# Kernel optimization log

Hardware: AMD Instinct MI355X
Metric: run time of the kernel (lower is better)

## Reference

```python
import jax, jax.numpy as jnp
import numpy as np

N = 50000   # nodes
E = 800000  # edges (avg degree 16)
IN = 384    # input gene features
H = 256     # hidden
EPS = 1e-12 # F.normalize eps


def setup_inputs() -> dict:
    key = jax.random.key(0)
    ks = jax.random.split(key, 10)
    x = jax.random.uniform(ks[0], (N, IN), dtype=jnp.float32) * 10.0  # count-like
    src = jax.random.randint(ks[1], (E,), 0, N, dtype=jnp.int32)
    dst = jax.random.randint(ks[2], (E,), 0, N, dtype=jnp.int32)
    def lin(k, din):
        return (jax.random.normal(k, (din, H), dtype=jnp.float32) / np.sqrt(din).astype(np.float32))
    return {
        'x': x, 'src': src, 'dst': dst,
        'W_self0': lin(ks[3], IN), 'W_neigh0': lin(ks[4], IN), 'b0': jnp.zeros((H,), jnp.float32),
        'W_self1': lin(ks[5], H), 'W_neigh1': lin(ks[6], H), 'b1': jnp.zeros((H,), jnp.float32),
        'W_self2': lin(ks[7], H), 'W_neigh2': lin(ks[8], H), 'b2': jnp.zeros((H,), jnp.float32),
    }


def _sage_mean(h, src, dst, Ws, Wn, b):
    # gather neighbor feats along edges, mean-aggregate into dst nodes
    msg = h[src]                                             # [E, d]
    agg = jax.ops.segment_sum(msg, dst, num_segments=N)      # [N, d]
    deg = jax.ops.segment_sum(jnp.ones((E,), h.dtype), dst, num_segments=N)
    h_neigh = agg / jnp.maximum(deg, 1.0)[:, None]           # isolated nodes -> 0
    return h @ Ws + h_neigh @ Wn + b


def _l2norm(h):
    n = jnp.sqrt(jnp.sum(h * h, axis=-1, keepdims=True))
    return h / jnp.maximum(n, EPS)


def reference(x, src, dst, W_self0, W_neigh0, b0, W_self1, W_neigh1, b1, W_self2, W_neigh2, b2):
    h = jnp.log1p(x)
    # layers 0..n-2: SAGEConv -> relu -> L2 normalize
    h = _l2norm(jax.nn.relu(_sage_mean(h, src, dst, W_self0, W_neigh0, b0)))
    h = _l2norm(jax.nn.relu(_sage_mean(h, src, dst, W_self1, W_neigh1, b1)))
    # last layer: plain SAGEConv (feat_drop inactive in eval)
    h = _sage_mean(h, src, dst, W_self2, W_neigh2, b2)
    return h
```

## Files before the change

### kernel.cpp

```cpp
#include <hip/hip_runtime.h>
#include <hip/hip_bf16.h>

#define N_NODES 50000
#define N_EDGES 800000
#define DIM_IN  384
#define DIM_H   256

typedef __bf16 bf16x8 __attribute__((ext_vector_type(8)));
typedef float  f32x4  __attribute__((ext_vector_type(4)));

static __device__ __forceinline__ ushort f2bf(float f) {
  uint u = __float_as_uint(f);
  u += 0x7fffu + ((u >> 16) & 1u);
  return (ushort)(u >> 16);
}
static __device__ __forceinline__ float bf_lo(uint u) { return __uint_as_float(u << 16); }
static __device__ __forceinline__ float bf_hi(uint u) { return __uint_as_float(u & 0xffff0000u); }

typedef const __attribute__((address_space(1))) void* gas_p;
typedef __attribute__((address_space(3))) void* las_p;
static __device__ __forceinline__ void gload16(const void* g, void* l) {
  __builtin_amdgcn_global_load_lds((gas_p)g, (las_p)l, 16, 0, 0);
}

static __device__ __forceinline__ float log1p_fast(float x) {
  return __logf(1.0f + x);
}

static __device__ __forceinline__ int permc(int p) {
  return ((p >> 7) << 7) + ((p & 7) << 4) + ((p >> 3) & 15);
}
static __device__ __forceinline__ void pack_one(const float* W, ushort* out, int local, bool perm) {
  int k = local >> 8, col = local & 255;
  int kc = k >> 5, kgd = (k >> 3) & 3, e = k & 7;
  int kgs = kgd ^ ((col >> 1) & 3);
  int krow = perm ? permc(k) : k;
  out[((size_t)kc * 256 + col) * 32 + kgs * 8 + e] = f2bf(W[krow * 256 + col]);
}

#define HIST_BLOCKS 3125
#define STRIPE1_TOT (HIST_BLOCKS * 7)
#define PACK_TOT (2 * DIM_IN * 256 + 4 * DIM_H * 256)
#define PACK_BLOCKS ((PACK_TOT + 255) / 256)

__global__ void prep_kernel(const float* __restrict__ x, ushort* __restrict__ h,
                            const int* __restrict__ dst, int* __restrict__ deg,
                            const float* W0s, const float* W0n, const float* W1s,
                            const float* W1n, const float* W2s, const float* W2n,
                            ushort* o0s, ushort* o0n, ushort* o1s, ushort* o1n,
                            ushort* o2s, ushort* o2n) {
  int bid = blockIdx.x;
  if (bid < STRIPE1_TOT) {
    int g = bid / 7, r = bid - g * 7;
    if (r == 0) {
      int i = g * 256 + threadIdx.x;
      if (i < N_EDGES) atomicAdd(&deg[dst[i]], 1);
    } else {
      int i = (g * 6 + (r - 1)) * 256 + threadIdx.x;
      float4 v = reinterpret_cast<const float4*>(x)[i];
      ushort4 o;
      o.x = f2bf(log1p_fast(v.x));
      o.y = f2bf(log1p_fast(v.y));
      o.z = f2bf(log1p_fast(v.z));
      o.w = f2bf(log1p_fast(v.w));
      reinterpret_cast<ushort4*>(h)[i] = o;
    }
  } else {
    int idx = (bid - STRIPE1_TOT) * 256 + threadIdx.x;
    const int SZ0 = DIM_IN * 256;
    const int SZ1 = DIM_H * 256;
    if (idx < SZ0) pack_one(W0s, o0s, idx, false);
    else if (idx < 2 * SZ0) pack_one(W0n, o0n, idx - SZ0, false);
    else if (idx < PACK_TOT) {
      int j = idx - 2 * SZ0;
      int w = j / SZ1, local = j - w * SZ1;
      if (w == 0) pack_one(W1s, o1s, local, true);
      else if (w == 1) pack_one(W1n, o1n, local, true);
      else if (w == 2) pack_one(W2s, o2s, local, true);
      else pack_one(W2n, o2n, local, true);
    }
  }
}

__global__ void scan1_kernel(const int* __restrict__ deg, int* __restrict__ tmp,
                             int* __restrict__ bsum) {
  __shared__ int buf[256];
  int t = threadIdx.x, i = blockIdx.x * 256 + t;
  int v = (i < N_NODES) ? deg[i] : 0;
  buf[t] = v;
  __syncthreads();
  int x = v;
#pragma unroll
  for (int off = 1; off < 256; off <<= 1) {
    int y = (t >= off) ? buf[t - off] : 0;
    __syncthreads();
    x += y;
    buf[t] = x;
    __syncthreads();
  }
  if (i < N_NODES) tmp[i] = x - v;
  if (t == 255) bsum[blockIdx.x] = x;
}

__global__ void scan2_kernel(int* __restrict__ bsum, int nb) {
  __shared__ int buf[256];
  int t = threadIdx.x;
  int v = (t < nb) ? bsum[t] : 0;
  buf[t] = v;
  __syncthreads();
  int x = v;
#pragma unroll
  for (int off = 1; off < 256; off <<= 1) {
    int y = (t >= off) ? buf[t - off] : 0;
    __syncthreads();
    x += y;
    buf[t] = x;
    __syncthreads();
  }
  if (t < nb) bsum[t] = x - v;
}

__global__ void scan3_kernel(const int* __restrict__ tmp, const int* __restrict__ bsum,
                             int* __restrict__ rowptr, int* __restrict__ cursor) {
  int i = blockIdx.x * 256 + threadIdx.x;
  if (i >= N_NODES) return;
  int r = tmp[i] + bsum[i >> 8];
  rowptr[i] = r;
  cursor[i] = r;
}

template <int K>
static __device__ void gemm_dual_body(int blk, ushort* Al, ushort* Bl, float* red,
                                      const ushort* __restrict__ A,
                                      const ushort* __restrict__ Bs,
                                      const ushort* __restrict__ Bn,
                                      const float* __restrict__ bias,
                                      ushort* __restrict__ Sout,
                                      unsigned char* __restrict__ Yq,
                                      float* __restrict__ scales) {
  constexpr int KC = K / 32;
  constexpr int NT = 2 * KC;
  const int tid = threadIdx.x;
  const int wv = tid >> 6, lane = tid & 63, lj = lane & 15, lg = lane >> 4;
  const int wm = wv >> 1, wn = wv & 1;
  const int r0 = blk * 128;

  int grow[2], akgd[2];
#pragma unroll
  for (int j = 0; j < 2; ++j) {
    int d = tid + j * 256;
    int row = d >> 2, kgs = d & 3;
    akgd[j] = kgs ^ ((row >> 1) & 3);
    int r = r0 + row;
    grow[j] = r < N_NODES ? r : N_NODES - 1;
  }

  int aoff[4], boff[8];
#pragma unroll
  for (int mf = 0; mf < 4; ++mf) {
    int row = wm * 64 + mf * 16 + lj;
    aoff[mf] = row * 32 + (lg ^ ((row >> 1) & 3)) * 8;
  }
#pragma unroll
  for (int f = 0; f < 8; ++f) {
    int col = wn * 128 + f * 16 + lj;
    boff[f] = col * 32 + (lg ^ ((col >> 1) & 3)) * 8;
  }

  auto stage = [&](int t, int bb) {
    int p = t >= KC;
    int kc = t - p * KC;
    const ushort* Bp = p ? Bn : Bs;
#pragma unroll
    for (int j = 0; j < 2; ++j)
      gload16(A + (size_t)grow[j] * K + kc * 32 + akgd[j] * 8,
              (char*)(Al + bb * 4096) + j * 4096 + wv * 1024);
#pragma unroll
    for (int j = 0; j < 4; ++j)
      gload16(Bp + (size_t)kc * 8192 + (tid + j * 256) * 8,
              (char*)(Bl + bb * 8192) + j * 4096 + wv * 1024);
  };

  float bvv[8];
#pragma unroll
  for (int f = 0; f < 8; ++f) bvv[f] = bias[wn * 128 + f * 16 + lj];

  f32x4 acc[4][8];
#pragma unroll
  for (int mf = 0; mf < 4; ++mf)
#pragma unroll
    for (int f = 0; f < 8; ++f) acc[mf][f] = (f32x4){0.f, 0.f, 0.f, 0.f};

  stage(0, 0);
  __syncthreads();
  int b = 0;
  for (int t = 0; t < NT; ++t) {
    if (t + 1 < NT) stage(t + 1, b ^ 1);
    bf16x8 av[4], bv[8];
#pragma unroll
    for (int mf = 0; mf < 4; ++mf)
      av[mf] = *reinterpret_cast<const bf16x8*>(Al + b * 4096 + aoff[mf]);
#pragma unroll
    for (int f = 0; f < 8; ++f)
      bv[f] = *reinterpret_cast<const bf16x8*>(Bl + b * 8192 + boff[f]);
#pragma unroll
    for (int mf = 0; mf < 4; ++mf)
#pragma unroll
      for (int f = 0; f < 8; ++f)
        acc[mf][f] = __builtin_amdgcn_mfma_f32_16x16x32_bf16(av[mf], bv[f], acc[mf][f], 0, 0, 0);
    if (t == KC - 1) {
#pragma unroll
      for (int mf = 0; mf < 4; ++mf)
#pragma unroll
        for (int e = 0; e < 4; ++e) {
          int row = r0 + wm * 64 + mf * 16 + lg * 4 + e;
          if (row < N_NODES) {
            ushort* pS = Sout + (size_t)row * 256 + wn * 128 + lj * 8;
            uint4 o;
            o.x = (uint)f2bf(acc[mf][0][e] + bvv[0]) | ((uint)f2bf(acc[mf][1][e] + bvv[1]) << 16);
            o.y = (uint)f2bf(acc[mf][2][e] + bvv[2]) | ((uint)f2bf(acc[mf][3][e] + bvv[3]) << 16);
            o.z = (uint)f2bf(acc[mf][4][e] + bvv[4]) | ((uint)f2bf(acc[mf][5][e] + bvv[5]) << 16);
            o.w = (uint)f2bf(acc[mf][6][e] + bvv[6]) | ((uint)f2bf(acc[mf][7][e] + bvv[7]) << 16);
            *reinterpret_cast<uint4*>(pS) = o;
          }
        }
#pragma unroll
      for (int mf = 0; mf < 4; ++mf)
#pragma unroll
        for (int f = 0; f < 8; ++f) acc[mf][f] = (f32x4){0.f, 0.f, 0.f, 0.f};
    }
    __syncthreads();
    b ^= 1;
  }

  float rmax[4][4];
#pragma unroll
  for (int mf = 0; mf < 4; ++mf)
#pragma unroll
    for (int e = 0; e < 4; ++e) {
      float m = 0.f;
#pragma unroll
      for (int f = 0; f < 8; ++f) m = fmaxf(m, fabsf(acc[mf][f][e]));
      m = fmaxf(m, __shfl_xor(m, 1));
      m = fmaxf(m, __shfl_xor(m, 2));
      m = fmaxf(m, __shfl_xor(m, 4));
      m = fmaxf(m, __shfl_xor(m, 8));
      rmax[mf][e] = m;
    }
  if (lj == 0) {
#pragma unroll
    for (int mf = 0; mf < 4; ++mf)
#pragma unroll
      for (int e = 0; e < 4; ++e)
        red[(wn * 2 + wm) * 64 + mf * 16 + lg * 4 + e] = rmax[mf][e];
  }
  __syncthreads();
#pragma unroll
  for (int mf = 0; mf < 4; ++mf)
#pragma unroll
    for (int e = 0; e < 4; ++e) {
      float m = fmaxf(fmaxf(red[(0 * 2 + wm) * 64 + mf * 16 + lg * 4 + e],
                            red[(1 * 2 + wm) * 64 + mf * 16 + lg * 4 + e]), 1e-30f);
      float inv_s = 127.0f / m;
      int row = r0 + wm * 64 + mf * 16 + lg * 4 + e;
      if (row < N_NODES) {
        uint lo = 0, hi = 0;
#pragma unroll
        for (int f = 0; f < 4; ++f) {
          int q = (int)rintf(acc[mf][f][e] * inv_s) + 128;
          q = max(0, min(255, q));
          lo |= (uint)q << (8 * f);
        }
#pragma unroll
        for (int f = 4; f < 8; ++f) {
          int q = (int)rintf(acc[mf][f][e] * inv_s) + 128;
          q = max(0, min(255, q));
          hi |= (uint)q << (8 * (f - 4));
        }
        *reinterpret_cast<uint2*>(Yq + (size_t)row * 256 + wn * 128 + lj * 8) = make_uint2(lo, hi);
        if (wn == 0 && lj == 0) scales[row] = m * (1.0f / 127.0f);
      }
    }
}

#define GEMM_BLOCKS ((N_NODES + 127) / 128)
#define GF_TOT (GEMM_BLOCKS * 3)

__global__ __launch_bounds__(256, 2) void gemm0_fill_kernel(
    const ushort* __restrict__ A, const ushort* __restrict__ Bs,
    const ushort* __restrict__ Bn, const float* __restrict__ bias,
    ushort* __restrict__ Sout, unsigned char* __restrict__ Yq, float* __restrict__ scales,
    const int* __restrict__ src, const int* __restrict__ dst,
    int* __restrict__ cursor, ushort* __restrict__ csr) {
  __shared__ ushort Al[2 * 4096];
  __shared__ ushort Bl[2 * 8192];
  __shared__ float red[256];
  int g = blockIdx.x / 3, r = blockIdx.x - g * 3;
  if (r == 0) {
    gemm_dual_body<DIM_IN>(g, Al, Bl, red, A, Bs, Bn, bias, Sout, Yq, scales);
  } else {
    int fb = g * 2 + (r - 1);
    int base = fb * 1024 + threadIdx.x * 4;
    if (base + 3 < N_EDGES) {
      int4 d4 = *reinterpret_cast<const int4*>(dst + base);
      int4 s4 = *reinterpret_cast<const int4*>(src + base);
      int p0 = atomicAdd(&cursor[d4.x], 1);
      int p1 = atomicAdd(&cursor[d4.y], 1);
      int p2 = atomicAdd(&cursor[d4.z], 1);
      int p3 = atomicAdd(&cursor[d4.w], 1);
      csr[p0] = (ushort)s4.x;
      csr[p1] = (ushort)s4.y;
      csr[p2] = (ushort)s4.z;
      csr[p3] = (ushort)s4.w;
    } else {
#pragma unroll
      for (int j = 0; j < 4; ++j) {
        int i = base + j;
        if (i < N_EDGES) {
          int d = dst[i];
          int p = atomicAdd(&cursor[d], 1);
          csr[p] = (ushort)src[i];
        }
      }
    }
  }
}

__global__ __launch_bounds__(256, 2) void gemm_dual_kernel(
    const ushort* __restrict__ A, const ushort* __restrict__ Bs,
    const ushort* __restrict__ Bn, const float* __restrict__ bias,
    ushort* __restrict__ Sout, unsigned char* __restrict__ Yq, float* __restrict__ scales) {
  __shared__ ushort Al[2 * 4096];
  __shared__ ushort Bl[2 * 8192];
  __shared__ float red[256];
  gemm_dual_body<DIM_H>(blockIdx.x, Al, Bl, red, A, Bs, Bn, bias, Sout, Yq, scales);
}

template <bool FINAL>
__global__ __launch_bounds__(256) void gather_kernel(const unsigned char* __restrict__ Yq,
                                                     const float* __restrict__ scales,
                                                     const ushort* __restrict__ Sin,
                                                     const int* __restrict__ rowptr,
                                                     const int* __restrict__ deg,
                                                     const ushort* __restrict__ csr,
                                                     void* __restrict__ outv) {
  int node = blockIdx.x * 8 + (threadIdx.x >> 5);
  if (node >= N_NODES) return;
  int hl = threadIdx.x & 31;
  int start = rowptr[node];
  int d = deg[node];
  float acc[8];
#pragma unroll
  for (int i = 0; i < 8; ++i) acc[i] = 0.0f;
  float stot = 0.f;

  auto ub = [](uint u, int j) { return (float)((u >> (8 * j)) & 0xffu); };
  int e = 0;
  for (; e + 4 <= d; e += 4) {
    int s0 = csr[start + e], s1 = csr[start + e + 1];
    int s2 = csr[start + e + 2], s3 = csr[start + e + 3];
    float c0 = scales[s0], c1 = scales[s1], c2 = scales[s2], c3 = scales[s3];
    uint2 q0 = *reinterpret_cast<const uint2*>(Yq + (size_t)s0 * 256 + hl * 8);
    uint2 q1 = *reinterpret_cast<const uint2*>(Yq + (size_t)s1 * 256 + hl * 8);
    uint2 q2 = *reinterpret_cast<const uint2*>(Yq + (size_t)s2 * 256 + hl * 8);
    uint2 q3 = *reinterpret_cast<const uint2*>(Yq + (size_t)s3 * 256 + hl * 8);
    stot += c0 + c1 + c2 + c3;
#pragma unroll
    for (int j = 0; j < 4; ++j) {
      acc[j]     += c0 * ub(q0.x, j) + c1 * ub(q1.x, j) + c2 * ub(q2.x, j) + c3 * ub(q3.x, j);
      acc[4 + j] += c0 * ub(q0.y, j) + c1 * ub(q1.y, j) + c2 * ub(q2.y, j) + c3 * ub(q3.y, j);
    }
  }
  for (; e < d; ++e) {
    int s = csr[start + e];
    float c = scales[s];
    uint2 q = *reinterpret_cast<const uint2*>(Yq + (size_t)s * 256 + hl * 8);
    stot += c;
#pragma unroll
    for (int j = 0; j < 4; ++j) {
      acc[j]     += c * ub(q.x, j);
      acc[4 + j] += c * ub(q.y, j);
    }
  }

  float invd = 1.0f / fmaxf((float)d, 1.0f);
  float nb[8];
#pragma unroll
  for (int j = 0; j < 8; ++j) nb[j] = (acc[j] - 128.0f * stot) * invd;

  uint4 sv = *reinterpret_cast<const uint4*>(Sin + (size_t)node * 256 + hl * 8);
  uint su[4] = {sv.x, sv.y, sv.z, sv.w};

  if constexpr (FINAL) {
    float* out = (float*)outv + (size_t)node * 256 + (hl >> 4) * 128 + (hl & 15);
#pragma unroll
    for (int i = 0; i < 4; ++i) {
      out[(2 * i) * 16]     = nb[2 * i] + bf_lo(su[i]);
      out[(2 * i + 1) * 16] = nb[2 * i + 1] + bf_hi(su[i]);
    }
  } else {
    float v[8];
    float ssq = 0.f;
#pragma unroll
    for (int i = 0; i < 4; ++i) {
      float a = fmaxf(nb[2 * i] + bf_lo(su[i]), 0.0f);
      float b = fmaxf(nb[2 * i + 1] + bf_hi(su[i]), 0.0f);
      v[2 * i] = a; v[2 * i + 1] = b;
      ssq += a * a + b * b;
    }
    ssq += __shfl_xor(ssq, 1);
    ssq += __shfl_xor(ssq, 2);
    ssq += __shfl_xor(ssq, 4);
    ssq += __shfl_xor(ssq, 8);
    ssq += __shfl_xor(ssq, 16);
    float rn = 1.0f / fmaxf(sqrtf(ssq), 1e-12f);
    uint o[4];
#pragma unroll
    for (int i = 0; i < 4; ++i) {
      uint lo = f2bf(v[2 * i] * rn);
      uint hi = f2bf(v[2 * i + 1] * rn);
      o[i] = lo | (hi << 16);
    }
    *reinterpret_cast<uint4*>((ushort*)outv + (size_t)node * 256 + hl * 8) =
        make_uint4(o[0], o[1], o[2], o[3]);
  }
}

extern "C" void kernel_launch(void* const* d_in, const int* in_sizes, int n_in,
                              void* d_out, int out_size, void* d_ws, size_t ws_size,
                              hipStream_t stream) {
  const float* x   = (const float*)d_in[0];
  const int*   src = (const int*)d_in[1];
  const int*   dst = (const int*)d_in[2];
  const float* Ws0 = (const float*)d_in[3];
  const float* Wn0 = (const float*)d_in[4];
  const float* b0  = (const float*)d_in[5];
  const float* Ws1 = (const float*)d_in[6];
  const float* Wn1 = (const float*)d_in[7];
  const float* b1  = (const float*)d_in[8];
  const float* Ws2 = (const float*)d_in[9];
  const float* Wn2 = (const float*)d_in[10];
  const float* b2  = (const float*)d_in[11];

  uintptr_t p = ((uintptr_t)d_ws + 255) & ~(uintptr_t)255;
  auto carve = [&](size_t bytes) {
    void* r = (void*)p;
    p += (bytes + 255) & ~(size_t)255;
    return r;
  };
  ushort* h0 = (ushort*)carve((size_t)N_NODES * DIM_IN * 2);
  ushort* h2 = h0;
  ushort* S_mid = (ushort*)carve((size_t)N_NODES * DIM_H * 2);
  ushort* h1 = (ushort*)carve((size_t)N_NODES * DIM_H * 2);
  unsigned char* Yq = (unsigned char*)carve((size_t)N_NODES * 256);
  float* scales = (float*)carve((size_t)N_NODES * 4);
  ushort* Ws0p = (ushort*)carve((size_t)DIM_IN * 256 * 2);
  ushort* Wn0p = (ushort*)carve((size_t)DIM_IN * 256 * 2);
  ushort* Ws1p = (ushort*)carve((size_t)DIM_H * 256 * 2);
  ushort* Wn1p = (ushort*)carve((size_t)DIM_H * 256 * 2);
  ushort* Ws2p = (ushort*)carve((size_t)DIM_H * 256 * 2);
  ushort* Wn2p = (ushort*)carve((size_t)DIM_H * 256 * 2);
  int* deg    = (int*)carve((size_t)N_NODES * 4);
  int* rowptr = (int*)carve((size_t)N_NODES * 4);
  int* cursor = (int*)carve((size_t)N_NODES * 4);
  int* stmp   = (int*)carve((size_t)N_NODES * 4);
  int* bsum   = (int*)carve(256 * 4);
  ushort* csr = (ushort*)carve((size_t)N_EDGES * 2);

  hipMemsetAsync(deg, 0, (size_t)N_NODES * 4, stream);

  prep_kernel<<<STRIPE1_TOT + PACK_BLOCKS, 256, 0, stream>>>(
      x, h0, dst, deg, Ws0, Wn0, Ws1, Wn1, Ws2, Wn2,
      Ws0p, Wn0p, Ws1p, Wn1p, Ws2p, Wn2p);

  const int scanBlocks = (N_NODES + 255) / 256;
  scan1_kernel<<<scanBlocks, 256, 0, stream>>>(deg, stmp, bsum);
  scan2_kernel<<<1, 256, 0, stream>>>(bsum, scanBlocks);
  scan3_kernel<<<scanBlocks, 256, 0, stream>>>(stmp, bsum, rowptr, cursor);

  gemm0_fill_kernel<<<GF_TOT, 256, 0, stream>>>(
      h0, Ws0p, Wn0p, b0, S_mid, Yq, scales, src, dst, cursor, csr);

  const int gatherBlocks = (N_NODES + 7) / 8;

  gather_kernel<false><<<gatherBlocks, 256, 0, stream>>>(Yq, scales, S_mid, rowptr, deg, csr, h1);
  gemm_dual_kernel<<<GEMM_BLOCKS, 256, 0, stream>>>(h1, Ws1p, Wn1p, b1, S_mid, Yq, scales);
  gather_kernel<false><<<gatherBlocks, 256, 0, stream>>>(Yq, scales, S_mid, rowptr, deg, csr, h2);
  gemm_dual_kernel<<<GEMM_BLOCKS, 256, 0, stream>>>(h2, Ws2p, Wn2p, b2, S_mid, Yq, scales);
  gather_kernel<true><<<gatherBlocks, 256, 0, stream>>>(Yq, scales, S_mid, rowptr, deg, csr, d_out);
}
```

Measured before the change: 300.4 us.

## Fuse log1p and bf16 conversion of input features into layer-0 GEMM staging

```diff
diff --git a/kernel.cpp b/kernel.cpp
--- a/kernel.cpp
+++ b/kernel.cpp
@@ -39,34 +39,20 @@
 }
 
 #define HIST_BLOCKS 3125
-#define STRIPE1_TOT (HIST_BLOCKS * 7)
 #define PACK_TOT (2 * DIM_IN * 256 + 4 * DIM_H * 256)
 #define PACK_BLOCKS ((PACK_TOT + 255) / 256)
 
-__global__ void prep_kernel(const float* __restrict__ x, ushort* __restrict__ h,
-                            const int* __restrict__ dst, int* __restrict__ deg,
+__global__ void prep_kernel(const int* __restrict__ dst, int* __restrict__ deg,
                             const float* W0s, const float* W0n, const float* W1s,
                             const float* W1n, const float* W2s, const float* W2n,
                             ushort* o0s, ushort* o0n, ushort* o1s, ushort* o1n,
                             ushort* o2s, ushort* o2n) {
   int bid = blockIdx.x;
-  if (bid < STRIPE1_TOT) {
-    int g = bid / 7, r = bid - g * 7;
-    if (r == 0) {
-      int i = g * 256 + threadIdx.x;
-      if (i < N_EDGES) atomicAdd(&deg[dst[i]], 1);
-    } else {
-      int i = (g * 6 + (r - 1)) * 256 + threadIdx.x;
-      float4 v = reinterpret_cast<const float4*>(x)[i];
-      ushort4 o;
-      o.x = f2bf(log1p_fast(v.x));
-      o.y = f2bf(log1p_fast(v.y));
-      o.z = f2bf(log1p_fast(v.z));
-      o.w = f2bf(log1p_fast(v.w));
-      reinterpret_cast<ushort4*>(h)[i] = o;
-    }
+  if (bid < HIST_BLOCKS) {
+    int i = bid * 256 + threadIdx.x;
+    if (i < N_EDGES) atomicAdd(&deg[dst[i]], 1);
   } else {
-    int idx = (bid - STRIPE1_TOT) * 256 + threadIdx.x;
+    int idx = (bid - HIST_BLOCKS) * 256 + threadIdx.x;
     const int SZ0 = DIM_IN * 256;
     const int SZ1 = DIM_H * 256;
     if (idx < SZ0) pack_one(W0s, o0s, idx, false);
@@ -129,9 +115,10 @@
   cursor[i] = r;
 }
 
-template <int K>
+template <int K, bool F32A>
 static __device__ void gemm_dual_body(int blk, ushort* Al, ushort* Bl, float* red,
                                       const ushort* __restrict__ A,
+                                      const float* __restrict__ Xf,
                                       const ushort* __restrict__ Bs,
                                       const ushort* __restrict__ Bn,
                                       const float* __restrict__ bias,
@@ -146,13 +133,18 @@
   const int r0 = blk * 128;
 
   int grow[2], akgd[2];
+  const float* sx[2];
+  int ldsoff[2];
 #pragma unroll
   for (int j = 0; j < 2; ++j) {
     int d = tid + j * 256;
-    int row = d >> 2, kgs = d & 3;
-    akgd[j] = kgs ^ ((row >> 1) & 3);
+    int row = d >> 2, kg = d & 3;
     int r = r0 + row;
-    grow[j] = r < N_NODES ? r : N_NODES - 1;
+    r = r < N_NODES ? r : N_NODES - 1;
+    akgd[j] = kg ^ ((row >> 1) & 3);
+    grow[j] = r;
+    sx[j] = Xf + (size_t)r * K + kg * 8;
+    ldsoff[j] = row * 32 + (kg ^ ((row >> 1) & 3)) * 8;
   }
 
   int aoff[4], boff[8];
@@ -172,13 +164,28 @@
     int kc = t - p * KC;
     const ushort* Bp = p ? Bn : Bs;
 #pragma unroll
-    for (int j = 0; j < 2; ++j)
-      gload16(A + (size_t)grow[j] * K + kc * 32 + akgd[j] * 8,
-              (char*)(Al + bb * 4096) + j * 4096 + wv * 1024);
-#pragma unroll
     for (int j = 0; j < 4; ++j)
       gload16(Bp + (size_t)kc * 8192 + (tid + j * 256) * 8,
               (char*)(Bl + bb * 8192) + j * 4096 + wv * 1024);
+    if constexpr (F32A) {
+#pragma unroll
+      for (int j = 0; j < 2; ++j) {
+        const float* s = sx[j] + kc * 32;
+        float4 a = *reinterpret_cast<const float4*>(s);
+        float4 b = *reinterpret_cast<const float4*>(s + 4);
+        uint4 o;
+        o.x = (uint)f2bf(log1p_fast(a.x)) | ((uint)f2bf(log1p_fast(a.y)) << 16);
+        o.y = (uint)f2bf(log1p_fast(a.z)) | ((uint)f2bf(log1p_fast(a.w)) << 16);
+        o.z = (uint)f2bf(log1p_fast(b.x)) | ((uint)f2bf(log1p_fast(b.y)) << 16);
+        o.w = (uint)f2bf(log1p_fast(b.z)) | ((uint)f2bf(log1p_fast(b.w)) << 16);
+        *reinterpret_cast<uint4*>(Al + bb * 4096 + ldsoff[j]) = o;
+      }
+    } else {
+#pragma unroll
+      for (int j = 0; j < 2; ++j)
+        gload16(A + (size_t)grow[j] * K + kc * 32 + akgd[j] * 8,
+                (char*)(Al + bb * 4096) + j * 4096 + wv * 1024);
+    }
   };
 
   float bvv[8];
@@ -195,7 +202,6 @@
   __syncthreads();
   int b = 0;
   for (int t = 0; t < NT; ++t) {
-    if (t + 1 < NT) stage(t + 1, b ^ 1);
     bf16x8 av[4], bv[8];
 #pragma unroll
     for (int mf = 0; mf < 4; ++mf)
@@ -203,6 +209,7 @@
 #pragma unroll
     for (int f = 0; f < 8; ++f)
       bv[f] = *reinterpret_cast<const bf16x8*>(Bl + b * 8192 + boff[f]);
+    if (t + 1 < NT) stage(t + 1, b ^ 1);
 #pragma unroll
     for (int mf = 0; mf < 4; ++mf)
 #pragma unroll
@@ -287,7 +294,7 @@
 #define GF_TOT (GEMM_BLOCKS * 3)
 
 __global__ __launch_bounds__(256, 2) void gemm0_fill_kernel(
-    const ushort* __restrict__ A, const ushort* __restrict__ Bs,
+    const float* __restrict__ x, const ushort* __restrict__ Bs,
     const ushort* __restrict__ Bn, const float* __restrict__ bias,
     ushort* __restrict__ Sout, unsigned char* __restrict__ Yq, float* __restrict__ scales,
     const int* __restrict__ src, const int* __restrict__ dst,
@@ -297,7 +304,7 @@
   __shared__ float red[256];
   int g = blockIdx.x / 3, r = blockIdx.x - g * 3;
   if (r == 0) {
-    gemm_dual_body<DIM_IN>(g, Al, Bl, red, A, Bs, Bn, bias, Sout, Yq, scales);
+    gemm_dual_body<DIM_IN, true>(g, Al, Bl, red, nullptr, x, Bs, Bn, bias, Sout, Yq, scales);
   } else {
     int fb = g * 2 + (r - 1);
     int base = fb * 1024 + threadIdx.x * 4;
@@ -333,7 +340,7 @@
   __shared__ ushort Al[2 * 4096];
   __shared__ ushort Bl[2 * 8192];
   __shared__ float red[256];
-  gemm_dual_body<DIM_H>(blockIdx.x, Al, Bl, red, A, Bs, Bn, bias, Sout, Yq, scales);
+  gemm_dual_body<DIM_H, false>(blockIdx.x, Al, Bl, red, A, nullptr, Bs, Bn, bias, Sout, Yq, scales);
 }
 
 template <bool FINAL>
@@ -448,10 +455,9 @@
     p += (bytes + 255) & ~(size_t)255;
     return r;
   };
-  ushort* h0 = (ushort*)carve((size_t)N_NODES * DIM_IN * 2);
-  ushort* h2 = h0;
   ushort* S_mid = (ushort*)carve((size_t)N_NODES * DIM_H * 2);
   ushort* h1 = (ushort*)carve((size_t)N_NODES * DIM_H * 2);
+  ushort* h2 = (ushort*)carve((size_t)N_NODES * DIM_H * 2);
   unsigned char* Yq = (unsigned char*)carve((size_t)N_NODES * 256);
   float* scales = (float*)carve((size_t)N_NODES * 4);
   ushort* Ws0p = (ushort*)carve((size_t)DIM_IN * 256 * 2);
@@ -469,8 +475,8 @@
 
   hipMemsetAsync(deg, 0, (size_t)N_NODES * 4, stream);
 
-  prep_kernel<<<STRIPE1_TOT + PACK_BLOCKS, 256, 0, stream>>>(
-      x, h0, dst, deg, Ws0, Wn0, Ws1, Wn1, Ws2, Wn2,
+  prep_kernel<<<HIST_BLOCKS + PACK_BLOCKS, 256, 0, stream>>>(
+      dst, deg, Ws0, Wn0, Ws1, Wn1, Ws2, Wn2,
       Ws0p, Wn0p, Ws1p, Wn1p, Ws2p, Wn2p);
 
   const int scanBlocks = (N_NODES + 255) / 256;
@@ -479,7 +485,7 @@
   scan3_kernel<<<scanBlocks, 256, 0, stream>>>(stmp, bsum, rowptr, cursor);
 
   gemm0_fill_kernel<<<GF_TOT, 256, 0, stream>>>(
-      h0, Ws0p, Wn0p, b0, S_mid, Yq, scales, src, dst, cursor, csr);
+      x, Ws0p, Wn0p, b0, S_mid, Yq, scales, src, dst, cursor, csr);
 
   const int gatherBlocks = (N_NODES + 7) / 8;
 
```

Measured after the change: 314.5 us. 4.7% more time.
